# Optimization experiments

Measured on AMD Instinct MI355X. Metric: run time of the kernel, lower is better.

Reference implementation:

```python
import jax, jax.numpy as jnp
import numpy as np

N, E, F = 50000, 800000, 96
ND, ED, GD = 32, 16, 8
STEPS = 3
CAT4, CAT3 = 4 * F, 3 * F


def _dense_init(key, fan_in, fan_out):
    return jax.random.normal(key, (fan_in, fan_out), dtype=jnp.float32) / np.sqrt(fan_in)


def _mlp(x, w1, b1, w2, b2):
    h = jax.nn.leaky_relu(x @ w1 + b1)  # leaky_relu between layers, none after last
    return h @ w2 + b2


def setup_inputs() -> dict:
    key = jax.random.key(0)
    ks = jax.random.split(key, 24)
    inp = {
        "nodes": jax.random.normal(ks[0], (N, ND), dtype=jnp.float32),
        "edges": jax.random.normal(ks[1], (E, ED), dtype=jnp.float32),
        "globals_": jax.random.normal(ks[2], (1, GD), dtype=jnp.float32),
        "senders": jax.random.randint(ks[3], (E,), 0, N, dtype=jnp.int32),
        "receivers": jax.random.randint(ks[4], (E,), 0, N, dtype=jnp.int32),
        # embedder (one Dense per feature set)
        "Wn": _dense_init(ks[5], ND, F), "bn": jnp.zeros((F,), jnp.float32),
        "We": _dense_init(ks[6], ED, F), "be": jnp.zeros((F,), jnp.float32),
        "Wg": _dense_init(ks[7], GD, F), "bg": jnp.zeros((F,), jnp.float32),
    }
    # per-step GN MLP params (distinct per message-passing step), stacked on axis 0
    def stack(kbase, fan_in):
        sub = jax.random.split(kbase, STEPS)
        return jnp.stack([_dense_init(k, fan_in, F) for k in sub])
    inp["ew1"] = stack(ks[8], CAT4); inp["eb1"] = jnp.zeros((STEPS, F), jnp.float32)
    inp["ew2"] = stack(ks[9], F);    inp["eb2"] = jnp.zeros((STEPS, F), jnp.float32)
    inp["nw1"] = stack(ks[10], CAT4); inp["nb1"] = jnp.zeros((STEPS, F), jnp.float32)
    inp["nw2"] = stack(ks[11], F);    inp["nb2"] = jnp.zeros((STEPS, F), jnp.float32)
    inp["gw1"] = stack(ks[12], CAT3); inp["gb1"] = jnp.zeros((STEPS, F), jnp.float32)
    inp["gw2"] = stack(ks[13], F);    inp["gb2"] = jnp.zeros((STEPS, F), jnp.float32)
    return inp


def reference(nodes, edges, globals_, senders, receivers,
              Wn, bn, We, be, Wg, bg,
              ew1, eb1, ew2, eb2,
              nw1, nb1, nw2, nb2,
              gw1, gb1, gw2, gb2):
    n = nodes @ Wn + bn          # [N, F]
    e = edges @ We + be          # [E, F]
    g = globals_ @ Wg + bg       # [1, F]
    num_nodes = n.shape[0]
    for s in range(ew1.shape[0]):
        # edge update: concat(edges, sender nodes, receiver nodes, globals)
        ge = jnp.broadcast_to(g, (e.shape[0], g.shape[1]))
        e = _mlp(jnp.concatenate([e, n[senders], n[receivers], ge], axis=-1),
                 ew1[s], eb1[s], ew2[s], eb2[s])
        # node update: concat(nodes, sum of edges by sender, sum by receiver, globals)
        sent = jax.ops.segment_sum(e, senders, num_segments=num_nodes)
        recv = jax.ops.segment_sum(e, receivers, num_segments=num_nodes)
        gn = jnp.broadcast_to(g, (num_nodes, g.shape[1]))
        n = _mlp(jnp.concatenate([n, sent, recv, gn], axis=-1),
                 nw1[s], nb1[s], nw2[s], nb2[s])
        # global update: concat(sum nodes, sum edges, globals) -- single graph
        g = _mlp(jnp.concatenate([n.sum(0, keepdims=True), e.sum(0, keepdims=True), g], axis=-1),
                 gw1[s], gb1[s], gw2[s], gb2[s])
    return n, e, g
```

## Files before the change

kernel.cpp:

```cpp
#include <hip/hip_runtime.h>

typedef unsigned short u16;
typedef unsigned int u32;

#define NN 50000
#define NE 800000
#define FD 96

typedef float f32x4 __attribute__((ext_vector_type(4)));
typedef __bf16 bf16x8 __attribute__((ext_vector_type(8)));
typedef u16 u16x8 __attribute__((ext_vector_type(8)));
typedef u16 u16x4 __attribute__((ext_vector_type(4)));

__device__ __forceinline__ float bf2f(u16 u) { return __uint_as_float(((u32)u) << 16); }
__device__ __forceinline__ u16 f2bf(float f) {
  u32 u = __float_as_uint(f);
  u += 0x7fffu + ((u >> 16) & 1u);
  return (u16)(u >> 16);
}

__device__ __forceinline__ f32x4 MFMA(u16x8 a, u16x8 b, f32x4 c) {
  return __builtin_amdgcn_mfma_f32_16x16x32_bf16(
      __builtin_bit_cast(bf16x8, a), __builtin_bit_cast(bf16x8, b), c, 0, 0, 0);
}

__global__ void gn_wprep(const float* __restrict__ ew1,
                         const float* __restrict__ nw1, const float* __restrict__ nw2,
                         u16* __restrict__ wt) {
  int gid = blockIdx.x * 256 + threadIdx.x;
  if (gid >= 6 * 3 * 9216) return;
  int b = gid / (3 * 9216);
  int rem = gid - b * 3 * 9216;
  int s = rem / 9216;
  int e = rem - s * 9216;
  int n = e / 96, k = e - n * 96;
  float v;
  switch (b) {
    case 0: v = ew1[s * 36864 + (96 + k) * 96 + n]; break;
    case 1: v = ew1[s * 36864 + (192 + k) * 96 + n]; break;
    case 2: v = nw1[s * 36864 + k * 96 + n]; break;
    case 3: v = nw1[s * 36864 + (96 + k) * 96 + n]; break;
    case 4: v = nw1[s * 36864 + (192 + k) * 96 + n]; break;
    default: v = nw2[s * 9216 + k * 96 + n]; break;
  }
  wt[gid] = f2bf(v);
}

__global__ void gn_wprep_frag(const float* __restrict__ ew1, const float* __restrict__ ew2,
                              u16* __restrict__ wf) {
  int gid = blockIdx.x * 256 + threadIdx.x;
  if (gid >= 2 * 3 * 9216) return;
  int b = gid / (3 * 9216);
  int rem = gid - b * 3 * 9216;
  int s = rem / 9216;
  int idx = rem - s * 9216;
  int j = idx & 7, lane = (idx >> 3) & 63, tkb = idx >> 9;
  int kb = tkb % 3, t = tkb / 3;
  int k = kb * 32 + (lane >> 4) * 8 + j;
  int n = t * 16 + (lane & 15);
  float v = (b == 0) ? ew1[s * 36864 + k * 96 + n] : ew2[s * 9216 + k * 96 + n];
  wf[gid] = f2bf(v);
}

__global__ __launch_bounds__(256) void gn_embed_e_mfma(
    const float* __restrict__ edges, const float* __restrict__ W,
    const float* __restrict__ b, const int* __restrict__ pos_s,
    u16* __restrict__ out) {
  __shared__ u16 WS[96][40];
  for (int i = threadIdx.x; i < 96 * 32; i += 256) {
    int n = i >> 5, k = i & 31;
    WS[n][k] = (k < 16) ? f2bf(W[k * 96 + n]) : (u16)0;
  }
  __syncthreads();
  const int wave = threadIdx.x >> 6, lane = threadIdx.x & 63;
  const int l15 = lane & 15, lhi = lane >> 4;
  #pragma unroll 1
  for (int grp = 0; grp < 2; grp++) {
    const long ec = (long)blockIdx.x * 128 + (wave * 2 + grp) * 16 + l15;
    const long dst = pos_s[ec];
    u16x8 xf = {0, 0, 0, 0, 0, 0, 0, 0};
    if (lhi < 2) {
      const float* er = edges + ec * 16 + lhi * 8;
      f32x4 e0 = *(const f32x4*)er;
      f32x4 e1 = *(const f32x4*)(er + 4);
      xf = (u16x8){f2bf(e0[0]), f2bf(e0[1]), f2bf(e0[2]), f2bf(e0[3]),
                   f2bf(e1[0]), f2bf(e1[1]), f2bf(e1[2]), f2bf(e1[3])};
    }
    #pragma unroll
    for (int t = 0; t < 6; t++) {
      u16x8 wf = *(const u16x8*)&WS[t * 16 + l15][lhi * 8];
      f32x4 acc = {};
      acc = MFMA(wf, xf, acc);
      f32x4 bv = *(const f32x4*)(b + t * 16 + lhi * 4);
      f32x4 ov = acc + bv;
      u16x4 r = {f2bf(ov[0]), f2bf(ov[1]), f2bf(ov[2]), f2bf(ov[3])};
      *(u16x4*)(out + dst * 96 + t * 16 + lhi * 4) = r;
    }
  }
}

__global__ __launch_bounds__(256) void gn_embed_n_mfma(
    const float* __restrict__ nodes, const float* __restrict__ W,
    const float* __restrict__ b, u16* __restrict__ out) {
  __shared__ u16 WS[96][40];
  for (int i = threadIdx.x; i < 96 * 32; i += 256) {
    int n = i >> 5, k = i & 31;
    WS[n][k] = f2bf(W[k * 96 + n]);
  }
  __syncthreads();
  const int wave = threadIdx.x >> 6, lane = threadIdx.x & 63;
  const int l15 = lane & 15, lhi = lane >> 4;
  #pragma unroll 1
  for (int grp = 0; grp < 2; grp++) {
    const int ncol = blockIdx.x * 128 + (wave * 2 + grp) * 16 + l15;
    const int nc = ncol < NN ? ncol : (NN - 1);
    const float* nr = nodes + (size_t)nc * 32 + lhi * 8;
    f32x4 e0 = *(const f32x4*)nr;
    f32x4 e1 = *(const f32x4*)(nr + 4);
    u16x8 xf = {f2bf(e0[0]), f2bf(e0[1]), f2bf(e0[2]), f2bf(e0[3]),
                f2bf(e1[0]), f2bf(e1[1]), f2bf(e1[2]), f2bf(e1[3])};
    if (ncol < NN) {
      #pragma unroll
      for (int t = 0; t < 6; t++) {
        u16x8 wf = *(const u16x8*)&WS[t * 16 + l15][lhi * 8];
        f32x4 acc = {};
        acc = MFMA(wf, xf, acc);
        f32x4 bv = *(const f32x4*)(b + t * 16 + lhi * 4);
        f32x4 ov = acc + bv;
        u16x4 r = {f2bf(ov[0]), f2bf(ov[1]), f2bf(ov[2]), f2bf(ov[3])};
        *(u16x4*)(out + (size_t)ncol * 96 + t * 16 + lhi * 4) = r;
      }
    }
  }
}

__global__ void gn_gembed(const float* __restrict__ g_in, const float* __restrict__ W,
                          const float* __restrict__ b, float* __restrict__ gbuf) {
  int f = threadIdx.x;
  if (f >= 96) return;
  float a = b[f];
  #pragma unroll
  for (int k = 0; k < 8; k++) a += g_in[k] * W[k * 96 + f];
  gbuf[f] = a;
}

__global__ void gn_hist(const int* __restrict__ snd, const int* __restrict__ rcv,
                        int* __restrict__ cs, int* __restrict__ cr) {
  int i = blockIdx.x * 256 + threadIdx.x;
  if (i >= NE) return;
  atomicAdd(&cs[snd[i]], 1);
  atomicAdd(&cr[rcv[i]], 1);
}

__global__ void gn_scan(const int* cnt, int* row_ptr, int* cursor, int n) {
  __shared__ int lsum[1024];
  int t = threadIdx.x;
  int chunk = (n + 1023) >> 10;
  int s0 = t * chunk;
  int s1 = s0 + chunk; if (s1 > n) s1 = n;
  int s = 0;
  for (int i = s0; i < s1; i++) s += cnt[i];
  lsum[t] = s;
  __syncthreads();
  for (int off = 1; off < 1024; off <<= 1) {
    int v = (t >= off) ? lsum[t - off] : 0;
    __syncthreads();
    lsum[t] += v;
    __syncthreads();
  }
  if (t == 0) row_ptr[n] = lsum[1023];
  int prefix = (t == 0) ? 0 : lsum[t - 1];
  for (int i = s0; i < s1; i++) {
    int c = cnt[i];
    row_ptr[i] = prefix;
    cursor[i] = prefix;
    prefix += c;
  }
}

__global__ void gn_scatter2(const int* __restrict__ snd, const int* __restrict__ rcv,
                            int* cur_s, int* cur_r,
                            int* __restrict__ el_s, int* __restrict__ pos_s,
                            int* __restrict__ el_r2,
                            int* __restrict__ snd_srt, int* __restrict__ rcv_srt) {
  int i = blockIdx.x * 256 + threadIdx.x;
  if (i >= NE) return;
  int s = snd[i], r = rcv[i];
  int p = atomicAdd(&cur_s[s], 1);
  int q = atomicAdd(&cur_r[r], 1);
  el_s[p] = i;
  pos_s[i] = p;
  el_r2[q] = p;
  snd_srt[p] = s;
  rcv_srt[p] = r;
}

__global__ void gn_segsum(const int* __restrict__ row_ptr, const int* __restrict__ el,
                          const u16* __restrict__ e, u16* __restrict__ out) {
  int node = blockIdx.x * 4 + (threadIdx.x >> 6);
  int w = threadIdx.x & 63;
  if (w >= 48) return;
  int beg = row_ptr[node], end = row_ptr[node + 1];
  float ax[8] = {}, ay[8] = {};
  int j = beg;
  for (; j + 8 <= end; j += 8) {
    u32 v[8];
    #pragma unroll
    for (int q = 0; q < 8; q++) v[q] = ((const u32*)(e + (size_t)el[j + q] * 96))[w];
    #pragma unroll
    for (int q = 0; q < 8; q++) {
      ax[q] += bf2f((u16)(v[q] & 0xffffu));
      ay[q] += bf2f((u16)(v[q] >> 16));
    }
  }
  for (; j < end; j++) {
    u32 v = ((const u32*)(e + (size_t)el[j] * 96))[w];
    ax[0] += bf2f((u16)(v & 0xffffu)); ay[0] += bf2f((u16)(v >> 16));
  }
  float sx = ((ax[0] + ax[1]) + (ax[2] + ax[3])) + ((ax[4] + ax[5]) + (ax[6] + ax[7]));
  float sy = ((ay[0] + ay[1]) + (ay[2] + ay[3])) + ((ay[4] + ay[5]) + (ay[6] + ay[7]));
  ((u32*)(out + (size_t)node * 96))[w] = (u32)f2bf(sx) | ((u32)f2bf(sy) << 16);
}

__global__ void gn_colsum(const u16* __restrict__ x, float* __restrict__ out, int M) {
  int w = threadIdx.x & 63;
  int rg = threadIdx.x >> 6;
  if (w >= 48) return;
  float ax = 0.f, ay = 0.f;
  for (int r = blockIdx.x * 4 + rg; r < M; r += gridDim.x * 4) {
    u32 v = ((const u32*)(x + (size_t)r * 96))[w];
    ax += bf2f((u16)(v & 0xffffu));
    ay += bf2f((u16)(v >> 16));
  }
  atomicAdd(&out[2 * w], ax);
  atomicAdd(&out[2 * w + 1], ay);
}

__global__ void gn_colsum32(const float* __restrict__ x, float* __restrict__ out, int M) {
  int w = threadIdx.x & 63;
  int rg = threadIdx.x >> 6;
  if (w >= 48) return;
  float ax = 0.f, ay = 0.f;
  for (int r = blockIdx.x * 4 + rg; r < M; r += gridDim.x * 4) {
    const float* row = x + (size_t)r * 96 + w * 2;
    ax += row[0];
    ay += row[1];
  }
  atomicAdd(&out[2 * w], ax);
  atomicAdd(&out[2 * w + 1], ay);
}

__global__ void gn_cvec(const float* __restrict__ g, const float* __restrict__ ew1,
                        const float* __restrict__ eb1, float* __restrict__ cve,
                        const float* __restrict__ nw1, const float* __restrict__ nb1,
                        float* __restrict__ cvn, int s) {
  int f = threadIdx.x;
  if (f >= 96) return;
  const float* W = (blockIdx.x == 0 ? ew1 : nw1) + s * 36864 + 288 * 96;
  const float* b = (blockIdx.x == 0 ? eb1 : nb1) + s * 96;
  float* o = blockIdx.x == 0 ? cve : cvn;
  float a = b[f];
  for (int k = 0; k < 96; k++) a += g[k] * W[k * 96 + f];
  o[f] = a;
}

__global__ __launch_bounds__(256) void gn_proj(const u16* __restrict__ n_in,
                                               const u16* __restrict__ wts, const u16* __restrict__ wtr,
                                               u16* __restrict__ ps, u16* __restrict__ pr) {
  __shared__ u16 WS[96][104];
  __shared__ u16 WR[96][104];
  for (int i = threadIdx.x; i < 96 * 48; i += 256) {
    int n = i / 48, k2 = (i - n * 48) * 2;
    *(u32*)&WS[n][k2] = ((const u32*)wts)[i];
    *(u32*)&WR[n][k2] = ((const u32*)wtr)[i];
  }
  __syncthreads();
  const int wave = threadIdx.x >> 6, lane = threadIdx.x & 63;
  const int l15 = lane & 15, lhi = lane >> 4;
  #pragma unroll 1
  for (int grp = 0; grp < 2; grp++) {
    const int gidx = wave * 2 + grp;
    const int ncol = blockIdx.x * 128 + gidx * 16 + l15;
    const int nc = ncol < NN ? ncol : (NN - 1);
    const u16* row = n_in + (size_t)nc * 96;
    u16x8 xf0 = *(const u16x8*)(row + 0 * 32 + lhi * 8);
    u16x8 xf1 = *(const u16x8*)(row + 1 * 32 + lhi * 8);
    u16x8 xf2 = *(const u16x8*)(row + 2 * 32 + lhi * 8);
    f32x4 a[6] = {}, b[6] = {};
    #pragma unroll
    for (int kb = 0; kb < 3; kb++) {
      u16x8 xf = (kb == 0) ? xf0 : ((kb == 1) ? xf1 : xf2);
      #pragma unroll
      for (int t = 0; t < 6; t++) {
        u16x8 wfa = *(const u16x8*)&WS[t * 16 + l15][kb * 32 + lhi * 8];
        u16x8 wfb = *(const u16x8*)&WR[t * 16 + l15][kb * 32 + lhi * 8];
        a[t] = MFMA(wfa, xf, a[t]);
        b[t] = MFMA(wfb, xf, b[t]);
      }
    }
    if (ncol < NN) {
      #pragma unroll
      for (int t = 0; t < 6; t++) {
        u16x4 ra = {f2bf(a[t][0]), f2bf(a[t][1]), f2bf(a[t][2]), f2bf(a[t][3])};
        u16x4 rb = {f2bf(b[t][0]), f2bf(b[t][1]), f2bf(b[t][2]), f2bf(b[t][3])};
        *(u16x4*)(ps + (size_t)ncol * 96 + t * 16 + lhi * 4) = ra;
        *(u16x4*)(pr + (size_t)ncol * 96 + t * 16 + lhi * 4) = rb;
      }
    }
  }
}

#define ETPW 2
#define SB_P 104
__global__ __launch_bounds__(512) void gn_edge3(
    u16* __restrict__ e_st,
    const u16* __restrict__ ps, const u16* __restrict__ pr,
    const int* __restrict__ snd, const int* __restrict__ rcv,
    const int* __restrict__ el_s,
    const float* __restrict__ cvec, const float* __restrict__ b2,
    const u16* __restrict__ wf1, const u16* __restrict__ wf2,
    float* __restrict__ sent32,
    float* __restrict__ out32) {
  __shared__ u16 W1[1152 * 8];
  __shared__ u16 W2[1152 * 8];
  __shared__ u16 Hb[8][16 * SB_P];
  for (int i = threadIdx.x; i < 1152; i += 512) {
    *(u16x8*)&W1[i * 8] = *(const u16x8*)(wf1 + (size_t)i * 8);
    *(u16x8*)&W2[i * 8] = *(const u16x8*)(wf2 + (size_t)i * 8);
  }
  __syncthreads();
  const int wave = threadIdx.x >> 6, lane = threadIdx.x & 63;
  const int l15 = lane & 15, lhi = lane >> 4;
  u16* myH = Hb[wave];
  const long t0 = ((long)blockIdx.x * 8 + wave) * ETPW;

  int r3[3], o3[3];
  #pragma unroll
  for (int s3 = 0; s3 < 3; s3++) { int g = s3 * 512 + lane * 8; r3[s3] = g / 96; o3[s3] = g - 96 * r3[s3]; }
  int r6[6], o6[6];
  #pragma unroll
  for (int s6 = 0; s6 < 6; s6++) { int g = s6 * 256 + lane * 4; r6[s6] = g / 96; o6[s6] = g - 96 * r6[s6]; }

  float ax = 0.f, ay = 0.f;

  u16x8 xf0, xf1, xf2;
  u16x4 ga[6], gb[6];
  u16x8 nxf0, nxf1, nxf2; int nsi = 0, nri = 0;
  u16x4 nga[6], ngb[6];

  {
    const u16* erow = e_st + (t0 * 16 + l15) * 96;
    xf0 = *(const u16x8*)(erow + lhi * 8);
    xf1 = *(const u16x8*)(erow + 32 + lhi * 8);
    xf2 = *(const u16x8*)(erow + 64 + lhi * 8);
    int si = snd[t0 * 16 + l15], ri = rcv[t0 * 16 + l15];
    const u16* pa = ps + (size_t)si * 96 + lhi * 4;
    const u16* pb = pr + (size_t)ri * 96 + lhi * 4;
    #pragma unroll
    for (int t = 0; t < 6; t++) { ga[t] = *(const u16x4*)(pa + t * 16); gb[t] = *(const u16x4*)(pb + t * 16); }
  }

  #pragma unroll 1
  for (int it = 0; it < ETPW; it++) {
    const long tb = (t0 + it) * 16;
    const long ecol = tb + l15;
    if (it + 1 < ETPW) {
      const u16* erow = e_st + (ecol + 16) * 96;
      nxf0 = *(const u16x8*)(erow + lhi * 8);
      nxf1 = *(const u16x8*)(erow + 32 + lhi * 8);
      nxf2 = *(const u16x8*)(erow + 64 + lhi * 8);
      nsi = snd[ecol + 16]; nri = rcv[ecol + 16];
    }
    f32x4 acc[6] = {};
    #pragma unroll
    for (int t = 0; t < 6; t++) acc[t] = MFMA(*(const u16x8*)&W1[((t * 3 + 0) * 64 + lane) * 8], xf0, acc[t]);
    #pragma unroll
    for (int t = 0; t < 6; t++) acc[t] = MFMA(*(const u16x8*)&W1[((t * 3 + 1) * 64 + lane) * 8], xf1, acc[t]);
    #pragma unroll
    for (int t = 0; t < 6; t++) acc[t] = MFMA(*(const u16x8*)&W1[((t * 3 + 2) * 64 + lane) * 8], xf2, acc[t]);
    if (it + 1 < ETPW) {
      const u16* pa = ps + (size_t)nsi * 96 + lhi * 4;
      const u16* pb = pr + (size_t)nri * 96 + lhi * 4;
      #pragma unroll
      for (int t = 0; t < 6; t++) { nga[t] = *(const u16x4*)(pa + t * 16); ngb[t] = *(const u16x4*)(pb + t * 16); }
    }
    asm volatile("s_waitcnt lgkmcnt(0)" ::: "memory");
    __builtin_amdgcn_sched_barrier(0);
    #pragma unroll
    for (int t = 0; t < 6; t++) {
      f32x4 cv = *(const f32x4*)(cvec + t * 16 + lhi * 4);
      u16x4 hp;
      #pragma unroll
      for (int j = 0; j < 4; j++) {
        float v = acc[t][j] + bf2f(ga[t][j]) + bf2f(gb[t][j]) + cv[j];
        v = v > 0.f ? v : 0.01f * v;
        hp[j] = f2bf(v);
      }
      int q = (4 * t + lhi) & 7;
      int kb2 = (4 * t + lhi) >> 3;
      *(u16x4*)&myH[(kb2 * 64 + (q >> 1) * 16 + l15) * 8 + (q & 1) * 4] = hp;
    }
    f32x4 o[6] = {};
    #pragma unroll
    for (int kb = 0; kb < 3; kb++) {
      u16x8 hf = *(const u16x8*)&myH[(kb * 64 + lane) * 8];
      #pragma unroll
      for (int t = 0; t < 6; t++)
        o[t] = MFMA(*(const u16x8*)&W2[((t * 3 + kb) * 64 + lane) * 8], hf, o[t]);
    }
    asm volatile("s_waitcnt lgkmcnt(0)" ::: "memory");
    __builtin_amdgcn_sched_barrier(0);
    #pragma unroll
    for (int t = 0; t < 6; t++) {
      f32x4 bv = *(const f32x4*)(b2 + t * 16 + lhi * 4);
      f32x4 ov = o[t] + bv;
      u16x4 r4 = {f2bf(ov[0]), f2bf(ov[1]), f2bf(ov[2]), f2bf(ov[3])};
      *(u16x4*)&myH[l15 * SB_P + t * 16 + lhi * 4] = r4;
    }
    asm volatile("s_waitcnt lgkmcnt(0)" ::: "memory");
    __builtin_amdgcn_sched_barrier(0);
    #pragma unroll
    for (int s3 = 0; s3 < 3; s3++) {
      u16x8 v = *(const u16x8*)&myH[r3[s3] * SB_P + o3[s3]];
      *(u16x8*)(e_st + tb * 96 + s3 * 512 + lane * 8) = v;
    }
    if (out32) {
      #pragma unroll
      for (int s6 = 0; s6 < 6; s6++) {
        long oc = el_s[tb + r6[s6]];
        u16x4 v = *(const u16x4*)&myH[r6[s6] * SB_P + o6[s6]];
        f32x4 f = {bf2f(v[0]), bf2f(v[1]), bf2f(v[2]), bf2f(v[3])};
        *(f32x4*)(out32 + oc * 96 + o6[s6]) = f;
      }
    }
    if (lane < 48) {
      #pragma unroll
      for (int r = 0; r < 16; r++) {
        u32 v = *(const u32*)&myH[r * SB_P + lane * 2];
        float lo = bf2f((u16)(v & 0xffffu)), hi = bf2f((u16)(v >> 16));
        ax += lo; ay += hi;
        int scur = snd[tb + r];
        bool flush;
        if (r < 15) flush = (snd[tb + r + 1] != scur);
        else flush = (it == ETPW - 1) || (snd[tb + 16] != scur);
        if (flush) {
          atomicAdd(&sent32[(size_t)scur * 96 + lane * 2], ax);
          atomicAdd(&sent32[(size_t)scur * 96 + lane * 2 + 1], ay);
          ax = 0.f; ay = 0.f;
        }
      }
    }
    xf0 = nxf0; xf1 = nxf1; xf2 = nxf2;
    #pragma unroll
    for (int t = 0; t < 6; t++) { ga[t] = nga[t]; gb[t] = ngb[t]; }
  }
}

__global__ __launch_bounds__(256) void gn_node(
    const u16* __restrict__ n_in, const float* __restrict__ sent32, const u16* __restrict__ recv,
    const u16* __restrict__ wta, const u16* __restrict__ wtb, const u16* __restrict__ wtc,
    const u16* __restrict__ wt2,
    const float* __restrict__ cvec, const float* __restrict__ b2,
    u16* __restrict__ n_out, float* __restrict__ out32) {
  __shared__ u16 WA[96][104];
  __shared__ u16 WB[96][104];
  __shared__ u16 Hb[4][16][104];
  for (int i = threadIdx.x; i < 96 * 48; i += 256) {
    int n = i / 48, k2 = (i - n * 48) * 2;
    *(u32*)&WA[n][k2] = ((const u32*)wta)[i];
    *(u32*)&WB[n][k2] = ((const u32*)wtb)[i];
  }
  __syncthreads();
  const int wave = threadIdx.x >> 6, lane = threadIdx.x & 63;
  const int l15 = lane & 15, lhi = lane >> 4;
  #pragma unroll 1
  for (int grp = 0; grp < 2; grp++) {
    const int gidx = wave * 2 + grp;
    const int ncol = blockIdx.x * 128 + gidx * 16 + l15;
    const int nc = ncol < NN ? ncol : (NN - 1);
    f32x4 acc[6] = {};
    {
      const u16* row = n_in + (size_t)nc * 96;
      #pragma unroll
      for (int kb = 0; kb < 3; kb++) {
        u16x8 xf = *(const u16x8*)(row + kb * 32 + lhi * 8);
        #pragma unroll
        for (int t = 0; t < 6; t++) {
          u16x8 wf = *(const u16x8*)&WA[t * 16 + l15][kb * 32 + lhi * 8];
          acc[t] = MFMA(wf, xf, acc[t]);
        }
      }
    }
    {
      const float* srow = sent32 + (size_t)nc * 96;
      #pragma unroll
      for (int kb = 0; kb < 3; kb++) {
        f32x4 a0 = *(const f32x4*)(srow + kb * 32 + lhi * 8);
        f32x4 a1 = *(const f32x4*)(srow + kb * 32 + lhi * 8 + 4);
        u16x8 xf = {f2bf(a0[0]), f2bf(a0[1]), f2bf(a0[2]), f2bf(a0[3]),
                    f2bf(a1[0]), f2bf(a1[1]), f2bf(a1[2]), f2bf(a1[3])};
        #pragma unroll
        for (int t = 0; t < 6; t++) {
          u16x8 wf = *(const u16x8*)&WB[t * 16 + l15][kb * 32 + lhi * 8];
          acc[t] = MFMA(wf, xf, acc[t]);
        }
      }
    }
    {
      const u16* row = recv + (size_t)nc * 96;
      #pragma unroll
      for (int kb = 0; kb < 3; kb++) {
        u16x8 xf = *(const u16x8*)(row + kb * 32 + lhi * 8);
        #pragma unroll
        for (int t = 0; t < 6; t++) {
          u16x8 wf = *(const u16x8*)(wtc + (t * 16 + l15) * 96 + kb * 32 + lhi * 8);
          acc[t] = MFMA(wf, xf, acc[t]);
        }
      }
    }
    #pragma unroll
    for (int t = 0; t < 6; t++) {
      f32x4 cv = *(const f32x4*)(cvec + t * 16 + lhi * 4);
      u16x4 hp;
      #pragma unroll
      for (int j = 0; j < 4; j++) {
        float v = acc[t][j] + cv[j];
        v = v > 0.f ? v : 0.01f * v;
        hp[j] = f2bf(v);
      }
      *(u16x4*)&Hb[wave][l15][t * 16 + lhi * 4] = hp;
    }
    f32x4 o[6] = {};
    #pragma unroll
    for (int kb = 0; kb < 3; kb++) {
      u16x8 hf = *(const u16x8*)&Hb[wave][l15][kb * 32 + lhi * 8];
      #pragma unroll
      for (int t = 0; t < 6; t++) {
        u16x8 wf = *(const u16x8*)(wt2 + (t * 16 + l15) * 96 + kb * 32 + lhi * 8);
        o[t] = MFMA(wf, hf, o[t]);
      }
    }
    if (ncol < NN) {
      #pragma unroll
      for (int t = 0; t < 6; t++) {
        f32x4 bv = *(const f32x4*)(b2 + t * 16 + lhi * 4);
        f32x4 ov = o[t] + bv;
        u16x4 r = {f2bf(ov[0]), f2bf(ov[1]), f2bf(ov[2]), f2bf(ov[3])};
        *(u16x4*)(n_out + (size_t)ncol * 96 + t * 16 + lhi * 4) = r;
        if (out32) *(f32x4*)(out32 + (size_t)ncol * 96 + t * 16 + lhi * 4) = ov;
      }
    }
  }
}

__global__ void gn_global(const float* __restrict__ nsum, const float* __restrict__ esum,
                          float* gbuf, const float* __restrict__ gw1, const float* __restrict__ gb1,
                          const float* __restrict__ gw2, const float* __restrict__ gb2,
                          int s, float* outg) {
  __shared__ float x[288];
  __shared__ float h[96];
  int t = threadIdx.x;
  if (t < 96) { x[t] = nsum[t]; x[96 + t] = esum[t]; x[192 + t] = gbuf[t]; }
  __syncthreads();
  if (t < 96) {
    const float* W1 = gw1 + s * 288 * 96;
    float a = gb1[s * 96 + t];
    for (int k = 0; k < 288; k++) a += x[k] * W1[k * 96 + t];
    h[t] = a > 0.f ? a : 0.01f * a;
  }
  __syncthreads();
  if (t < 96) {
    const float* W2 = gw2 + s * 9216;
    float a = gb2[s * 96 + t];
    for (int k = 0; k < 96; k++) a += h[k] * W2[k * 96 + t];
    gbuf[t] = a;
    if (outg) outg[t] = a;
  }
}

extern "C" void kernel_launch(void* const* d_in, const int* in_sizes, int n_in,
                              void* d_out, int out_size, void* d_ws, size_t ws_size,
                              hipStream_t stream) {
  (void)in_sizes; (void)n_in; (void)out_size;
  const float* nodes    = (const float*)d_in[0];
  const float* edges    = (const float*)d_in[1];
  const float* globals_ = (const float*)d_in[2];
  const int*   senders  = (const int*)d_in[3];
  const int*   receivers= (const int*)d_in[4];
  const float* Wn = (const float*)d_in[5],  *bn = (const float*)d_in[6];
  const float* We = (const float*)d_in[7],  *be = (const float*)d_in[8];
  const float* Wg = (const float*)d_in[9],  *bg = (const float*)d_in[10];
  const float* ew1 = (const float*)d_in[11], *eb1 = (const float*)d_in[12];
  const float* ew2 = (const float*)d_in[13], *eb2 = (const float*)d_in[14];
  const float* nw1 = (const float*)d_in[15], *nb1 = (const float*)d_in[16];
  const float* nw2 = (const float*)d_in[17], *nb2 = (const float*)d_in[18];
  const float* gw1 = (const float*)d_in[19], *gb1 = (const float*)d_in[20];
  const float* gw2 = (const float*)d_in[21], *gb2 = (const float*)d_in[22];

  size_t off = 0;
  char* base = (char*)d_ws;
  auto A = [&](size_t bytes) -> void* {
    void* p = base + off;
    off = (off + bytes + 255) & ~(size_t)255;
    return p;
  };
  u16* e_bf    = (u16*)A((size_t)NE * FD * 2);
  u16* n_bf    = (u16*)A((size_t)NN * FD * 2);
  u16* ps      = (u16*)A((size_t)NN * FD * 2);
  u16* pr      = (u16*)A((size_t)NN * FD * 2);
  u16* recv    = (u16*)A((size_t)NN * FD * 2);
  float* sent32= (float*)A((size_t)NN * FD * 4);
  u16* wt_all  = (u16*)A((size_t)6 * 3 * 9216 * 2);
  u16* wf_all  = (u16*)A((size_t)2 * 3 * 9216 * 2);
  int* row_s   = (int*)A((size_t)(NN + 1) * 4);
  int* row_r   = (int*)A((size_t)(NN + 1) * 4);
  int* el_s    = (int*)A((size_t)NE * 4);
  int* el_r2   = (int*)A((size_t)NE * 4);
  int* pos_s   = (int*)A((size_t)NE * 4);
  int* snd_srt = (int*)A((size_t)NE * 4);
  int* rcv_srt = (int*)A((size_t)NE * 4);
  int* cur_s   = (int*)A((size_t)NN * 4);
  int* cur_r   = (int*)A((size_t)NN * 4);
  float* gbuf   = (float*)A(96 * 4);
  float* cvec_e = (float*)A(96 * 4);
  float* cvec_n = (float*)A(96 * 4);
  float* sums   = (float*)A(2 * 96 * 4);
  if (off > ws_size) return;

  float* out_n = (float*)d_out;
  float* out_e = out_n + (size_t)NN * FD;
  float* out_g = out_n + (size_t)NN * FD + (size_t)NE * FD;

  auto WT = [&](int b, int s) { return wt_all + (size_t)(b * 3 + s) * 9216; };

  gn_wprep<<<648, 256, 0, stream>>>(ew1, nw1, nw2, wt_all);
  gn_wprep_frag<<<216, 256, 0, stream>>>(ew1, ew2, wf_all);
  gn_embed_n_mfma<<<(NN + 127) / 128, 256, 0, stream>>>(nodes, Wn, bn, n_bf);
  gn_gembed<<<1, 128, 0, stream>>>(globals_, Wg, bg, gbuf);

  hipMemsetAsync(cur_s, 0, (size_t)NN * 4, stream);
  hipMemsetAsync(cur_r, 0, (size_t)NN * 4, stream);
  gn_hist<<<(NE + 255) / 256, 256, 0, stream>>>(senders, receivers, cur_s, cur_r);
  gn_scan<<<1, 1024, 0, stream>>>(cur_s, row_s, cur_s, NN);
  gn_scan<<<1, 1024, 0, stream>>>(cur_r, row_r, cur_r, NN);
  gn_scatter2<<<(NE + 255) / 256, 256, 0, stream>>>(senders, receivers, cur_s, cur_r,
                                                    el_s, pos_s, el_r2, snd_srt, rcv_srt);
  gn_embed_e_mfma<<<NE / 128, 256, 0, stream>>>(edges, We, be, pos_s, e_bf);

  const int eblocks = NE / (16 * 8 * ETPW);

  for (int s = 0; s < 3; s++) {
    bool last = (s == 2);
    hipMemsetAsync(sums, 0, 2 * 96 * 4, stream);
    hipMemsetAsync(sent32, 0, (size_t)NN * FD * 4, stream);
    gn_cvec<<<2, 128, 0, stream>>>(gbuf, ew1, eb1, cvec_e, nw1, nb1, cvec_n, s);
    gn_proj<<<(NN + 127) / 128, 256, 0, stream>>>(n_bf, WT(0, s), WT(1, s), ps, pr);
    gn_edge3<<<eblocks, 512, 0, stream>>>(e_bf, ps, pr, snd_srt, rcv_srt, el_s,
                                          cvec_e, eb2 + s * 96,
                                          wf_all + (size_t)s * 9216,
                                          wf_all + (size_t)(3 + s) * 9216,
                                          sent32,
                                          last ? out_e : (float*)nullptr);
    gn_segsum<<<NN / 4, 256, 0, stream>>>(row_r, el_r2, e_bf, recv);
    gn_colsum32<<<256, 256, 0, stream>>>(sent32, sums + 96, NN);
    gn_node<<<(NN + 127) / 128, 256, 0, stream>>>(n_bf, sent32, recv,
                                                  WT(2, s), WT(3, s), WT(4, s), WT(5, s),
                                                  cvec_n, nb2 + s * 96, n_bf,
                                                  last ? out_n : (float*)nullptr);
    gn_colsum<<<256, 256, 0, stream>>>(n_bf, sums, NN);
    gn_global<<<1, 128, 0, stream>>>(sums, sums + 96, gbuf, gw1, gb1, gw2, gb2, s,
                                     last ? out_g : (float*)nullptr);
  }
}
```

Measured before the change: 1.881 ms.

## Fuse receiver segment-sum into edge kernel via fp32 atomics, shrink edge blocks

The separate receiver-side segment-sum kernel is removed. Each edge's output is now atomically added into an fp32 recv buffer inside the edge kernel, and the node kernel reads that buffer and converts it to bf16. The edge kernel also drops to 256 threads with a launch bound of 5 blocks, and W2 is read from global memory instead of being staged in LDS, which cuts LDS use to allow more resident blocks. In exchange the edge kernel issues 2 float atomics per element per edge with scattered receivers, adds an extra memset, and its W2 MFMA operands become global loads.

```diff
diff --git a/kernel.cpp b/kernel.cpp
--- a/kernel.cpp
+++ b/kernel.cpp
@@ -195,33 +195,6 @@
   rcv_srt[p] = r;
 }
 
-__global__ void gn_segsum(const int* __restrict__ row_ptr, const int* __restrict__ el,
-                          const u16* __restrict__ e, u16* __restrict__ out) {
-  int node = blockIdx.x * 4 + (threadIdx.x >> 6);
-  int w = threadIdx.x & 63;
-  if (w >= 48) return;
-  int beg = row_ptr[node], end = row_ptr[node + 1];
-  float ax[8] = {}, ay[8] = {};
-  int j = beg;
-  for (; j + 8 <= end; j += 8) {
-    u32 v[8];
-    #pragma unroll
-    for (int q = 0; q < 8; q++) v[q] = ((const u32*)(e + (size_t)el[j + q] * 96))[w];
-    #pragma unroll
-    for (int q = 0; q < 8; q++) {
-      ax[q] += bf2f((u16)(v[q] & 0xffffu));
-      ay[q] += bf2f((u16)(v[q] >> 16));
-    }
-  }
-  for (; j < end; j++) {
-    u32 v = ((const u32*)(e + (size_t)el[j] * 96))[w];
-    ax[0] += bf2f((u16)(v & 0xffffu)); ay[0] += bf2f((u16)(v >> 16));
-  }
-  float sx = ((ax[0] + ax[1]) + (ax[2] + ax[3])) + ((ax[4] + ax[5]) + (ax[6] + ax[7]));
-  float sy = ((ay[0] + ay[1]) + (ay[2] + ay[3])) + ((ay[4] + ay[5]) + (ay[6] + ay[7]));
-  ((u32*)(out + (size_t)node * 96))[w] = (u32)f2bf(sx) | ((u32)f2bf(sy) << 16);
-}
-
 __global__ void gn_colsum(const u16* __restrict__ x, float* __restrict__ out, int M) {
   int w = threadIdx.x & 63;
   int rg = threadIdx.x >> 6;
@@ -312,27 +285,24 @@
 
 #define ETPW 2
 #define SB_P 104
-__global__ __launch_bounds__(512) void gn_edge3(
+__global__ __launch_bounds__(256, 5) void gn_edge4(
     u16* __restrict__ e_st,
     const u16* __restrict__ ps, const u16* __restrict__ pr,
     const int* __restrict__ snd, const int* __restrict__ rcv,
     const int* __restrict__ el_s,
     const float* __restrict__ cvec, const float* __restrict__ b2,
     const u16* __restrict__ wf1, const u16* __restrict__ wf2,
-    float* __restrict__ sent32,
+    float* __restrict__ sent32, float* __restrict__ recv32,
     float* __restrict__ out32) {
   __shared__ u16 W1[1152 * 8];
-  __shared__ u16 W2[1152 * 8];
-  __shared__ u16 Hb[8][16 * SB_P];
-  for (int i = threadIdx.x; i < 1152; i += 512) {
+  __shared__ u16 Hb[4][16 * SB_P];
+  for (int i = threadIdx.x; i < 1152; i += 256)
     *(u16x8*)&W1[i * 8] = *(const u16x8*)(wf1 + (size_t)i * 8);
-    *(u16x8*)&W2[i * 8] = *(const u16x8*)(wf2 + (size_t)i * 8);
-  }
   __syncthreads();
   const int wave = threadIdx.x >> 6, lane = threadIdx.x & 63;
   const int l15 = lane & 15, lhi = lane >> 4;
   u16* myH = Hb[wave];
-  const long t0 = ((long)blockIdx.x * 8 + wave) * ETPW;
+  const long t0 = ((long)blockIdx.x * 4 + wave) * ETPW;
 
   int r3[3], o3[3];
   #pragma unroll
@@ -406,7 +376,7 @@
       u16x8 hf = *(const u16x8*)&myH[(kb * 64 + lane) * 8];
       #pragma unroll
       for (int t = 0; t < 6; t++)
-        o[t] = MFMA(*(const u16x8*)&W2[((t * 3 + kb) * 64 + lane) * 8], hf, o[t]);
+        o[t] = MFMA(*(const u16x8*)(wf2 + ((size_t)(t * 3 + kb) * 64 + lane) * 8), hf, o[t]);
     }
     asm volatile("s_waitcnt lgkmcnt(0)" ::: "memory");
     __builtin_amdgcn_sched_barrier(0);
@@ -438,6 +408,9 @@
       for (int r = 0; r < 16; r++) {
         u32 v = *(const u32*)&myH[r * SB_P + lane * 2];
         float lo = bf2f((u16)(v & 0xffffu)), hi = bf2f((u16)(v >> 16));
+        int rcur = rcv[tb + r];
+        atomicAdd(&recv32[(size_t)rcur * 96 + lane * 2], lo);
+        atomicAdd(&recv32[(size_t)rcur * 96 + lane * 2 + 1], hi);
         ax += lo; ay += hi;
         int scur = snd[tb + r];
         bool flush;
@@ -457,7 +430,7 @@
 }
 
 __global__ __launch_bounds__(256) void gn_node(
-    const u16* __restrict__ n_in, const float* __restrict__ sent32, const u16* __restrict__ recv,
+    const u16* __restrict__ n_in, const float* __restrict__ sent32, const float* __restrict__ recv32,
     const u16* __restrict__ wta, const u16* __restrict__ wtb, const u16* __restrict__ wtc,
     const u16* __restrict__ wt2,
     const float* __restrict__ cvec, const float* __restrict__ b2,
@@ -507,10 +480,13 @@
       }
     }
     {
-      const u16* row = recv + (size_t)nc * 96;
+      const float* rrow = recv32 + (size_t)nc * 96;
       #pragma unroll
       for (int kb = 0; kb < 3; kb++) {
-        u16x8 xf = *(const u16x8*)(row + kb * 32 + lhi * 8);
+        f32x4 a0 = *(const f32x4*)(rrow + kb * 32 + lhi * 8);
+        f32x4 a1 = *(const f32x4*)(rrow + kb * 32 + lhi * 8 + 4);
+        u16x8 xf = {f2bf(a0[0]), f2bf(a0[1]), f2bf(a0[2]), f2bf(a0[3]),
+                    f2bf(a1[0]), f2bf(a1[1]), f2bf(a1[2]), f2bf(a1[3])};
         #pragma unroll
         for (int t = 0; t < 6; t++) {
           u16x8 wf = *(const u16x8*)(wtc + (t * 16 + l15) * 96 + kb * 32 + lhi * 8);
@@ -608,8 +584,8 @@
   u16* n_bf    = (u16*)A((size_t)NN * FD * 2);
   u16* ps      = (u16*)A((size_t)NN * FD * 2);
   u16* pr      = (u16*)A((size_t)NN * FD * 2);
-  u16* recv    = (u16*)A((size_t)NN * FD * 2);
   float* sent32= (float*)A((size_t)NN * FD * 4);
+  float* recv32= (float*)A((size_t)NN * FD * 4);
   u16* wt_all  = (u16*)A((size_t)6 * 3 * 9216 * 2);
   u16* wf_all  = (u16*)A((size_t)2 * 3 * 9216 * 2);
   int* row_s   = (int*)A((size_t)(NN + 1) * 4);
@@ -647,23 +623,23 @@
                                                     el_s, pos_s, el_r2, snd_srt, rcv_srt);
   gn_embed_e_mfma<<<NE / 128, 256, 0, stream>>>(edges, We, be, pos_s, e_bf);
 
-  const int eblocks = NE / (16 * 8 * ETPW);
+  const int eblocks = NE / (16 * 4 * ETPW);
 
   for (int s = 0; s < 3; s++) {
     bool last = (s == 2);
     hipMemsetAsync(sums, 0, 2 * 96 * 4, stream);
     hipMemsetAsync(sent32, 0, (size_t)NN * FD * 4, stream);
+    hipMemsetAsync(recv32, 0, (size_t)NN * FD * 4, stream);
     gn_cvec<<<2, 128, 0, stream>>>(gbuf, ew1, eb1, cvec_e, nw1, nb1, cvec_n, s);
     gn_proj<<<(NN + 127) / 128, 256, 0, stream>>>(n_bf, WT(0, s), WT(1, s), ps, pr);
-    gn_edge3<<<eblocks, 512, 0, stream>>>(e_bf, ps, pr, snd_srt, rcv_srt, el_s,
+    gn_edge4<<<eblocks, 256, 0, stream>>>(e_bf, ps, pr, snd_srt, rcv_srt, el_s,
                                           cvec_e, eb2 + s * 96,
                                           wf_all + (size_t)s * 9216,
                                           wf_all + (size_t)(3 + s) * 9216,
-                                          sent32,
+                                          sent32, recv32,
                                           last ? out_e : (float*)nullptr);
-    gn_segsum<<<NN / 4, 256, 0, stream>>>(row_r, el_r2, e_bf, recv);
     gn_colsum32<<<256, 256, 0, stream>>>(sent32, sums + 96, NN);
-    gn_node<<<(NN + 127) / 128, 256, 0, stream>>>(n_bf, sent32, recv,
+    gn_node<<<(NN + 127) / 128, 256, 0, stream>>>(n_bf, sent32, recv32,
                                                   WT(2, s), WT(3, s), WT(4, s), WT(5, s),
                                                   cvec_n, nb2 + s * 96, n_bf,
                                                   last ? out_n : (float*)nullptr);
```

New measurement: 3.334 ms. 1.77x slower.

## Replace atomic sender-sum in edge kernel with sequential segment-sum pass

Applied to the files above, without the earlier changes.

Removes the fused fp32 atomic accumulation of sender sums from the edge MLP kernel. It now computes those sums in a separate kernel that reads contiguous sender-sorted edge rows, so no index indirection is needed, and stores them as bf16. This drops the per-step memset of a large fp32 buffer and the atomics, and halves the traffic the node kernel reads for that input. The cost is one extra full read of the edge features. Edges per wave are raised from 2 to 5, which also lowers the block count.

```diff
diff --git a/kernel.cpp b/kernel.cpp
--- a/kernel.cpp
+++ b/kernel.cpp
@@ -195,6 +195,33 @@
   rcv_srt[p] = r;
 }
 
+__global__ void gn_segsum_seq(const int* __restrict__ row_ptr,
+                              const u16* __restrict__ e, u16* __restrict__ out) {
+  int node = blockIdx.x * 4 + (threadIdx.x >> 6);
+  int w = threadIdx.x & 63;
+  if (w >= 48) return;
+  int beg = row_ptr[node], end = row_ptr[node + 1];
+  float ax[8] = {}, ay[8] = {};
+  int j = beg;
+  for (; j + 8 <= end; j += 8) {
+    u32 v[8];
+    #pragma unroll
+    for (int q = 0; q < 8; q++) v[q] = ((const u32*)(e + (size_t)(j + q) * 96))[w];
+    #pragma unroll
+    for (int q = 0; q < 8; q++) {
+      ax[q] += bf2f((u16)(v[q] & 0xffffu));
+      ay[q] += bf2f((u16)(v[q] >> 16));
+    }
+  }
+  for (; j < end; j++) {
+    u32 v = ((const u32*)(e + (size_t)j * 96))[w];
+    ax[0] += bf2f((u16)(v & 0xffffu)); ay[0] += bf2f((u16)(v >> 16));
+  }
+  float sx = ((ax[0] + ax[1]) + (ax[2] + ax[3])) + ((ax[4] + ax[5]) + (ax[6] + ax[7]));
+  float sy = ((ay[0] + ay[1]) + (ay[2] + ay[3])) + ((ay[4] + ay[5]) + (ay[6] + ay[7]));
+  ((u32*)(out + (size_t)node * 96))[w] = (u32)f2bf(sx) | ((u32)f2bf(sy) << 16);
+}
+
 __global__ void gn_segsum(const int* __restrict__ row_ptr, const int* __restrict__ el,
                           const u16* __restrict__ e, u16* __restrict__ out) {
   int node = blockIdx.x * 4 + (threadIdx.x >> 6);
@@ -231,20 +258,6 @@
     u32 v = ((const u32*)(x + (size_t)r * 96))[w];
     ax += bf2f((u16)(v & 0xffffu));
     ay += bf2f((u16)(v >> 16));
-  }
-  atomicAdd(&out[2 * w], ax);
-  atomicAdd(&out[2 * w + 1], ay);
-}
-
-__global__ void gn_colsum32(const float* __restrict__ x, float* __restrict__ out, int M) {
-  int w = threadIdx.x & 63;
-  int rg = threadIdx.x >> 6;
-  if (w >= 48) return;
-  float ax = 0.f, ay = 0.f;
-  for (int r = blockIdx.x * 4 + rg; r < M; r += gridDim.x * 4) {
-    const float* row = x + (size_t)r * 96 + w * 2;
-    ax += row[0];
-    ay += row[1];
   }
   atomicAdd(&out[2 * w], ax);
   atomicAdd(&out[2 * w + 1], ay);
@@ -310,16 +323,15 @@
   }
 }
 
-#define ETPW 2
+#define ETPW 5
 #define SB_P 104
-__global__ __launch_bounds__(512) void gn_edge3(
+__global__ __launch_bounds__(512) void gn_edge5(
     u16* __restrict__ e_st,
     const u16* __restrict__ ps, const u16* __restrict__ pr,
     const int* __restrict__ snd, const int* __restrict__ rcv,
     const int* __restrict__ el_s,
     const float* __restrict__ cvec, const float* __restrict__ b2,
     const u16* __restrict__ wf1, const u16* __restrict__ wf2,
-    float* __restrict__ sent32,
     float* __restrict__ out32) {
   __shared__ u16 W1[1152 * 8];
   __shared__ u16 W2[1152 * 8];
@@ -340,8 +352,6 @@
   int r6[6], o6[6];
   #pragma unroll
   for (int s6 = 0; s6 < 6; s6++) { int g = s6 * 256 + lane * 4; r6[s6] = g / 96; o6[s6] = g - 96 * r6[s6]; }
-
-  float ax = 0.f, ay = 0.f;
 
   u16x8 xf0, xf1, xf2;
   u16x4 ga[6], gb[6];
@@ -433,23 +443,6 @@
         *(f32x4*)(out32 + oc * 96 + o6[s6]) = f;
       }
     }
-    if (lane < 48) {
-      #pragma unroll
-      for (int r = 0; r < 16; r++) {
-        u32 v = *(const u32*)&myH[r * SB_P + lane * 2];
-        float lo = bf2f((u16)(v & 0xffffu)), hi = bf2f((u16)(v >> 16));
-        ax += lo; ay += hi;
-        int scur = snd[tb + r];
-        bool flush;
-        if (r < 15) flush = (snd[tb + r + 1] != scur);
-        else flush = (it == ETPW - 1) || (snd[tb + 16] != scur);
-        if (flush) {
-          atomicAdd(&sent32[(size_t)scur * 96 + lane * 2], ax);
-          atomicAdd(&sent32[(size_t)scur * 96 + lane * 2 + 1], ay);
-          ax = 0.f; ay = 0.f;
-        }
-      }
-    }
     xf0 = nxf0; xf1 = nxf1; xf2 = nxf2;
     #pragma unroll
     for (int t = 0; t < 6; t++) { ga[t] = nga[t]; gb[t] = ngb[t]; }
@@ -457,7 +450,7 @@
 }
 
 __global__ __launch_bounds__(256) void gn_node(
-    const u16* __restrict__ n_in, const float* __restrict__ sent32, const u16* __restrict__ recv,
+    const u16* __restrict__ n_in, const u16* __restrict__ sent, const u16* __restrict__ recv,
     const u16* __restrict__ wta, const u16* __restrict__ wtb, const u16* __restrict__ wtc,
     const u16* __restrict__ wt2,
     const float* __restrict__ cvec, const float* __restrict__ b2,
@@ -492,13 +485,10 @@
       }
     }
     {
-      const float* srow = sent32 + (size_t)nc * 96;
+      const u16* row = sent + (size_t)nc * 96;
       #pragma unroll
       for (int kb = 0; kb < 3; kb++) {
-        f32x4 a0 = *(const f32x4*)(srow + kb * 32 + lhi * 8);
-        f32x4 a1 = *(const f32x4*)(srow + kb * 32 + lhi * 8 + 4);
-        u16x8 xf = {f2bf(a0[0]), f2bf(a0[1]), f2bf(a0[2]), f2bf(a0[3]),
-                    f2bf(a1[0]), f2bf(a1[1]), f2bf(a1[2]), f2bf(a1[3])};
+        u16x8 xf = *(const u16x8*)(row + kb * 32 + lhi * 8);
         #pragma unroll
         for (int t = 0; t < 6; t++) {
           u16x8 wf = *(const u16x8*)&WB[t * 16 + l15][kb * 32 + lhi * 8];
@@ -608,8 +598,8 @@
   u16* n_bf    = (u16*)A((size_t)NN * FD * 2);
   u16* ps      = (u16*)A((size_t)NN * FD * 2);
   u16* pr      = (u16*)A((size_t)NN * FD * 2);
+  u16* sent    = (u16*)A((size_t)NN * FD * 2);
   u16* recv    = (u16*)A((size_t)NN * FD * 2);
-  float* sent32= (float*)A((size_t)NN * FD * 4);
   u16* wt_all  = (u16*)A((size_t)6 * 3 * 9216 * 2);
   u16* wf_all  = (u16*)A((size_t)2 * 3 * 9216 * 2);
   int* row_s   = (int*)A((size_t)(NN + 1) * 4);
@@ -652,18 +642,17 @@
   for (int s = 0; s < 3; s++) {
     bool last = (s == 2);
     hipMemsetAsync(sums, 0, 2 * 96 * 4, stream);
-    hipMemsetAsync(sent32, 0, (size_t)NN * FD * 4, stream);
     gn_cvec<<<2, 128, 0, stream>>>(gbuf, ew1, eb1, cvec_e, nw1, nb1, cvec_n, s);
     gn_proj<<<(NN + 127) / 128, 256, 0, stream>>>(n_bf, WT(0, s), WT(1, s), ps, pr);
-    gn_edge3<<<eblocks, 512, 0, stream>>>(e_bf, ps, pr, snd_srt, rcv_srt, el_s,
+    gn_edge5<<<eblocks, 512, 0, stream>>>(e_bf, ps, pr, snd_srt, rcv_srt, el_s,
                                           cvec_e, eb2 + s * 96,
                                           wf_all + (size_t)s * 9216,
                                           wf_all + (size_t)(3 + s) * 9216,
-                                          sent32,
                                           last ? out_e : (float*)nullptr);
+    gn_segsum_seq<<<NN / 4, 256, 0, stream>>>(row_s, e_bf, sent);
     gn_segsum<<<NN / 4, 256, 0, stream>>>(row_r, el_r2, e_bf, recv);
-    gn_colsum32<<<256, 256, 0, stream>>>(sent32, sums + 96, NN);
-    gn_node<<<(NN + 127) / 128, 256, 0, stream>>>(n_bf, sent32, recv,
+    gn_colsum<<<256, 256, 0, stream>>>(sent, sums + 96, NN);
+    gn_node<<<(NN + 127) / 128, 256, 0, stream>>>(n_bf, sent, recv,
                                                   WT(2, s), WT(3, s), WT(4, s), WT(5, s),
                                                   cvec_n, nb2 + s * 96, n_bf,
                                                   last ? out_n : (float*)nullptr);
```

After: 1.676 ms. -10.9%, faster.
